# Kernel optimization log

Hardware: AMD Instinct MI355X
Metric: run time of the kernel (lower is better)

## Reference

```python
import jax, jax.numpy as jnp
import numpy as np

HEAD_DIM = 64
MASK_PENALTY = 1000000.0


def setup_inputs() -> dict:
    key = jax.random.key(0)
    kq, kk, kv, ki = jax.random.split(key, 4)
    B, H, S, D = 32, 16, 512, HEAD_DIM
    E, CAP = 8, 4  # n_experts = hidden(1024)//128, capacity per expert
    Q = jax.random.normal(kq, (B, H, S, D), dtype=jnp.float32)
    K = jax.random.normal(kk, (B, H, S, D), dtype=jnp.float32)
    V = jax.random.normal(kv, (B, H, S, D), dtype=jnp.float32)
    idx_list = jax.random.randint(ki, (E, CAP), 0, B)  # per-expert routed batch indices
    mask = jnp.ones((B, S), dtype=jnp.float32)
    return {"Q": Q, "K": K, "V": V, "idx_list": idx_list, "mask": mask}


def reference(Q, K, V, idx_list, mask):
    # Per-expert grouped attention: gather routed batch rows, QK^T, masked
    # softmax, AV. Dropout is identity in eval mode.
    scale = 1.0 / jnp.sqrt(jnp.asarray(HEAD_DIM, dtype=Q.dtype))

    def expert_attn(idx_e):
        q = Q[idx_e]            # [cap, H, S, D]
        k = K[idx_e]
        v = V[idx_e]
        m = mask[idx_e]         # [cap, S]
        dot = jnp.einsum('bhsd,bhtd->bhst', q, k) * scale
        dot = dot - MASK_PENALTY * (1.0 - m[:, None, None, :])
        p = jax.nn.softmax(dot, axis=-1)
        return jnp.einsum('bhst,bhtd->bhsd', p, v)  # [cap, H, S, D]

    X = jax.vmap(expert_attn)(idx_list)  # [E, cap, H, S, D]
    return X
```

## Files before the change

### kernel.cpp

```cpp
#include <hip/hip_runtime.h>
#include <math.h>


typedef _Float16 f16x8 __attribute__((ext_vector_type(8)));
typedef _Float16 f16x4 __attribute__((ext_vector_type(4)));
typedef _Float16 f16x2 __attribute__((ext_vector_type(2)));
typedef float    f32x4 __attribute__((ext_vector_type(4)));

#define MFMA16(a, b, c) __builtin_amdgcn_mfma_f32_16x16x32_f16((a), (b), (c), 0, 0, 0)

constexpr int Hh = 16;
constexpr int Ss = 512;
constexpr int Dd = 64;
constexpr int QB = 128;
constexpr int KVB = 64;
constexpr int NT = Ss / KVB;
constexpr float QS = 0.125f * 1.44269504088896f;
constexpr float BM = 1000000.0f * 1.44269504088896f;

union U8 { f16x8 v; f16x2 h[4]; };

__device__ __forceinline__ int SW(int row, int col) {
  return row * 64 + (col ^ ((row & 7) << 3));
}

__device__ __forceinline__ f16x2 pkrtz(float a, float b) {
  auto t = __builtin_amdgcn_cvt_pkrtz(a, b);
  return *(f16x2*)&t;
}

__global__ __launch_bounds__(256) void sparse_attn_kernel(
    const float* __restrict__ Q, const float* __restrict__ K,
    const float* __restrict__ V, const int* __restrict__ idx,
    const float* __restrict__ mask, float* __restrict__ out) {
  const int tid  = threadIdx.x;
  const int lane = tid & 63;
  const int wv   = tid >> 6;
  const int r    = lane & 15;
  const int g    = lane >> 4;

  const int phys = blockIdx.x;
  const int G    = (phys & 7) | ((phys >> 5) << 3);
  const int qb   = (phys >> 3) & 3;
  const int h    = G & 15;
  const int ec   = G >> 4;
  const int b    = idx[ec];

  __shared__ _Float16 Ks[2][64 * 64];
  __shared__ _Float16 VTs[2][64 * 64];
  __shared__ float    maskS[Ss];

  const size_t bh = ((size_t)b * Hh + h) * (size_t)Ss * Dd;
  const float* Qb = Q + bh;
  const float* Kb = K + bh;
  const float* Vb = V + bh;
  const float* mrow = mask + (size_t)b * Ss;

  *(float2*)&maskS[2 * tid] = *(const float2*)(mrow + 2 * tid);

  const int q0 = qb * QB + wv * 32;

  f16x8 qf[2][2];
#pragma unroll
  for (int mi = 0; mi < 2; ++mi)
#pragma unroll
    for (int kk = 0; kk < 2; ++kk) {
      const float* qp = Qb + (size_t)(q0 + mi * 16 + r) * Dd + kk * 32 + g * 8;
      float4 x0 = *(const float4*)qp;
      float4 x1 = *(const float4*)(qp + 4);
      U8 u;
      u.h[0] = pkrtz(x0.x * QS, x0.y * QS);
      u.h[1] = pkrtz(x0.z * QS, x0.w * QS);
      u.h[2] = pkrtz(x1.x * QS, x1.y * QS);
      u.h[3] = pkrtz(x1.z * QS, x1.w * QS);
      qf[mi][kk] = u.v;
    }

  f16x8 ones;
#pragma unroll
  for (int e = 0; e < 8; ++e) ones[e] = (_Float16)1.0f;

  f32x4 oacc[2][4];
#pragma unroll
  for (int mi = 0; mi < 2; ++mi)
#pragma unroll
    for (int nj = 0; nj < 4; ++nj) oacc[mi][nj] = (f32x4){0.f, 0.f, 0.f, 0.f};
  f32x4 lacc[2] = {(f32x4){0.f, 0.f, 0.f, 0.f}, (f32x4){0.f, 0.f, 0.f, 0.f}};

  float4 kx0[2], kx1[2];
  float  vv[2][8];

#define KV_ISSUE(KV0)                                                        \
  {                                                                          \
    _Pragma("unroll")                                                        \
    for (int it = 0; it < 2; ++it) {                                         \
      int j = it * 256 + tid;                                                \
      const float* kp_ = Kb + (size_t)((KV0) + (j >> 3)) * Dd + (j & 7) * 8; \
      kx0[it] = *(const float4*)kp_;                                         \
      kx1[it] = *(const float4*)(kp_ + 4);                                   \
    }                                                                        \
    _Pragma("unroll")                                                        \
    for (int it = 0; it < 2; ++it) {                                         \
      int oct = (tid >> 6) + 4 * it;                                         \
      int kb1 = (oct >> 2) * 16 + (oct & 3) * 4;                             \
      const float* vp = Vb + (size_t)((KV0) + kb1) * Dd + (tid & 63);        \
      _Pragma("unroll")                                                      \
      for (int jj = 0; jj < 4; ++jj) {                                       \
        vv[it][jj]     = vp[(size_t)jj * Dd];                                \
        vv[it][jj + 4] = vp[(size_t)(jj + 32) * Dd];                         \
      }                                                                      \
    }                                                                        \
  }

#define STAGE_WRITE(B)                                                       \
  {                                                                          \
    _Pragma("unroll")                                                        \
    for (int it = 0; it < 2; ++it) {                                         \
      int j = it * 256 + tid;                                                \
      U8 u;                                                                  \
      u.h[0] = pkrtz(kx0[it].x, kx0[it].y);                                  \
      u.h[1] = pkrtz(kx0[it].z, kx0[it].w);                                  \
      u.h[2] = pkrtz(kx1[it].x, kx1[it].y);                                  \
      u.h[3] = pkrtz(kx1[it].z, kx1[it].w);                                  \
      *(f16x8*)&Ks[B][SW(j >> 3, (j & 7) * 8)] = u.v;                        \
    }                                                                        \
    _Pragma("unroll")                                                        \
    for (int it = 0; it < 2; ++it) {                                         \
      int oct = (tid >> 6) + 4 * it;                                         \
      int dim = tid & 63;                                                    \
      U8 u;                                                                  \
      u.h[0] = pkrtz(vv[it][0], vv[it][1]);                                  \
      u.h[1] = pkrtz(vv[it][2], vv[it][3]);                                  \
      u.h[2] = pkrtz(vv[it][4], vv[it][5]);                                  \
      u.h[3] = pkrtz(vv[it][6], vv[it][7]);                                  \
      *(f16x8*)&VTs[B][SW(dim, oct * 8)] = u.v;                              \
    }                                                                        \
  }

  KV_ISSUE(0)
  STAGE_WRITE(0)
  __syncthreads();

  int cur = 0;
  for (int t = 0; t < NT; ++t) {
    const int kv0 = t * KVB;

    if (t < NT - 1) KV_ISSUE(kv0 + KVB)

    f32x4 bv[4];
#pragma unroll
    for (int nj = 0; nj < 4; ++nj) {
      f32x4 mv = *(const f32x4*)&maskS[kv0 + nj * 16 + g * 4];
      bv[nj][0] = mv[0] * BM - BM;
      bv[nj][1] = mv[1] * BM - BM;
      bv[nj][2] = mv[2] * BM - BM;
      bv[nj][3] = mv[3] * BM - BM;
    }

    f32x4 sf[2][4];
#pragma unroll
    for (int nj = 0; nj < 4; ++nj) { sf[0][nj] = bv[nj]; sf[1][nj] = bv[nj]; }
    __builtin_amdgcn_s_setprio(1);
#pragma unroll
    for (int nj = 0; nj < 4; ++nj)
#pragma unroll
      for (int kk = 0; kk < 2; ++kk) {
        f16x8 kf = *(const f16x8*)&Ks[cur][SW(nj * 16 + r, kk * 32 + g * 8)];
        sf[0][nj] = MFMA16(kf, qf[0][kk], sf[0][nj]);
        sf[1][nj] = MFMA16(kf, qf[1][kk], sf[1][nj]);
      }
    __builtin_amdgcn_s_setprio(0);

    f16x8 pf[2][2];
#pragma unroll
    for (int mi = 0; mi < 2; ++mi) {
      float p[4][4];
#pragma unroll
      for (int nj = 0; nj < 4; ++nj)
#pragma unroll
        for (int rg = 0; rg < 4; ++rg)
          p[nj][rg] = __builtin_amdgcn_exp2f(sf[mi][nj][rg]);
#pragma unroll
      for (int kk = 0; kk < 2; ++kk) {
        U8 u;
        u.h[0] = pkrtz(p[kk][0], p[kk][1]);
        u.h[1] = pkrtz(p[kk][2], p[kk][3]);
        u.h[2] = pkrtz(p[kk + 2][0], p[kk + 2][1]);
        u.h[3] = pkrtz(p[kk + 2][2], p[kk + 2][3]);
        pf[mi][kk] = u.v;
      }
    }

    __builtin_amdgcn_s_setprio(1);
#pragma unroll
    for (int kk = 0; kk < 2; ++kk) {
      lacc[0] = MFMA16(pf[0][kk], ones, lacc[0]);
      lacc[1] = MFMA16(pf[1][kk], ones, lacc[1]);
#pragma unroll
      for (int nj = 0; nj < 4; ++nj) {
        f16x8 vf = *(const f16x8*)&VTs[cur][SW(nj * 16 + r, kk * 32 + g * 8)];
        oacc[0][nj] = MFMA16(pf[0][kk], vf, oacc[0][nj]);
        oacc[1][nj] = MFMA16(pf[1][kk], vf, oacc[1][nj]);
      }
    }
    __builtin_amdgcn_s_setprio(0);

    if (t < NT - 1) {
      STAGE_WRITE(cur ^ 1)
      __syncthreads();
    }
    cur ^= 1;
  }

  float* ob = out + ((size_t)ec * Hh + h) * (size_t)Ss * Dd;
#pragma unroll
  for (int mi = 0; mi < 2; ++mi) {
    float i4[4];
#pragma unroll
    for (int rg = 0; rg < 4; ++rg) i4[rg] = 1.0f / lacc[mi][rg];
#pragma unroll
    for (int nj = 0; nj < 4; ++nj)
#pragma unroll
      for (int rg = 0; rg < 4; ++rg) {
        int row = q0 + mi * 16 + g * 4 + rg;
        int dim = nj * 16 + r;
        ob[(size_t)row * Dd + dim] = oacc[mi][nj][rg] * i4[rg];
      }
  }
}

extern "C" void kernel_launch(void* const* d_in, const int* in_sizes, int n_in,
                              void* d_out, int out_size, void* d_ws, size_t ws_size,
                              hipStream_t stream) {
  const float* Q    = (const float*)d_in[0];
  const float* K    = (const float*)d_in[1];
  const float* V    = (const float*)d_in[2];
  const int*   idx  = (const int*)d_in[3];
  const float* mask = (const float*)d_in[4];
  float* out = (float*)d_out;
  dim3 grid(2048), block(256);
  hipLaunchKernelGGL(sparse_attn_kernel, grid, block, 0, stream,
                     Q, K, V, idx, mask, out);
}
```

Baseline: 67.93 us.

## Use 256-row query blocks with 512 threads and single-buffered 128-row KV tiles

Each block now covers 256 query rows with 8 waves and 512 threads, so the grid halves and each K/V tile loaded from global memory is shared by twice as many queries. KV tiles grow to 128 rows and are held in a single LDS buffer. The next tile's global loads are issued into registers right after the current tile is written to LDS, and compute runs in two 64-key halves. The mask bias is precomputed once into shared memory. The cost is one extra barrier per tile, fewer blocks to spread across CUs, and higher register pressure under the 512-thread launch bound.

```diff
diff --git a/kernel.cpp b/kernel.cpp
--- a/kernel.cpp
+++ b/kernel.cpp
@@ -12,16 +12,19 @@
 constexpr int Hh = 16;
 constexpr int Ss = 512;
 constexpr int Dd = 64;
-constexpr int QB = 128;
-constexpr int KVB = 64;
-constexpr int NT = Ss / KVB;
+constexpr int QB = 256;
+constexpr int KVR = 128;
+constexpr int NR = Ss / KVR;
 constexpr float QS = 0.125f * 1.44269504088896f;
 constexpr float BM = 1000000.0f * 1.44269504088896f;
 
 union U8 { f16x8 v; f16x2 h[4]; };
 
-__device__ __forceinline__ int SW(int row, int col) {
+__device__ __forceinline__ int SW64(int row, int col) {
   return row * 64 + (col ^ ((row & 7) << 3));
+}
+__device__ __forceinline__ int SW128(int row, int col) {
+  return row * 128 + (col ^ ((row & 7) << 3));
 }
 
 __device__ __forceinline__ f16x2 pkrtz(float a, float b) {
@@ -29,7 +32,7 @@
   return *(f16x2*)&t;
 }
 
-__global__ __launch_bounds__(256) void sparse_attn_kernel(
+__global__ __launch_bounds__(512) void sparse_attn_kernel(
     const float* __restrict__ Q, const float* __restrict__ K,
     const float* __restrict__ V, const int* __restrict__ idx,
     const float* __restrict__ mask, float* __restrict__ out) {
@@ -40,15 +43,15 @@
   const int g    = lane >> 4;
 
   const int phys = blockIdx.x;
-  const int G    = (phys & 7) | ((phys >> 5) << 3);
-  const int qb   = (phys >> 3) & 3;
+  const int G    = (phys & 7) | ((phys >> 4) << 3);
+  const int qb   = (phys >> 3) & 1;
   const int h    = G & 15;
   const int ec   = G >> 4;
   const int b    = idx[ec];
 
-  __shared__ _Float16 Ks[2][64 * 64];
-  __shared__ _Float16 VTs[2][64 * 64];
-  __shared__ float    maskS[Ss];
+  __shared__ _Float16 Ks[128 * 64];
+  __shared__ _Float16 VTs[64 * 128];
+  __shared__ float    biasS[Ss];
 
   const size_t bh = ((size_t)b * Hh + h) * (size_t)Ss * Dd;
   const float* Qb = Q + bh;
@@ -56,7 +59,7 @@
   const float* Vb = V + bh;
   const float* mrow = mask + (size_t)b * Ss;
 
-  *(float2*)&maskS[2 * tid] = *(const float2*)(mrow + 2 * tid);
+  biasS[tid] = mrow[tid] * BM - BM;
 
   const int q0 = qb * QB + wv * 32;
 
@@ -94,15 +97,15 @@
   {                                                                          \
     _Pragma("unroll")                                                        \
     for (int it = 0; it < 2; ++it) {                                         \
-      int j = it * 256 + tid;                                                \
+      int j = it * 512 + tid;                                                \
       const float* kp_ = Kb + (size_t)((KV0) + (j >> 3)) * Dd + (j & 7) * 8; \
       kx0[it] = *(const float4*)kp_;                                         \
       kx1[it] = *(const float4*)(kp_ + 4);                                   \
     }                                                                        \
     _Pragma("unroll")                                                        \
     for (int it = 0; it < 2; ++it) {                                         \
-      int oct = (tid >> 6) + 4 * it;                                         \
-      int kb1 = (oct >> 2) * 16 + (oct & 3) * 4;                             \
+      int oct = tid >> 6;                                                    \
+      int kb1 = (oct >> 2) * 16 + (oct & 3) * 4 + it * 64;                   \
       const float* vp = Vb + (size_t)((KV0) + kb1) * Dd + (tid & 63);        \
       _Pragma("unroll")                                                      \
       for (int jj = 0; jj < 4; ++jj) {                                       \
@@ -112,104 +115,100 @@
     }                                                                        \
   }
 
-#define STAGE_WRITE(B)                                                       \
+#define STAGE_WRITE()                                                        \
   {                                                                          \
     _Pragma("unroll")                                                        \
     for (int it = 0; it < 2; ++it) {                                         \
-      int j = it * 256 + tid;                                                \
+      int j = it * 512 + tid;                                                \
       U8 u;                                                                  \
       u.h[0] = pkrtz(kx0[it].x, kx0[it].y);                                  \
       u.h[1] = pkrtz(kx0[it].z, kx0[it].w);                                  \
       u.h[2] = pkrtz(kx1[it].x, kx1[it].y);                                  \
       u.h[3] = pkrtz(kx1[it].z, kx1[it].w);                                  \
-      *(f16x8*)&Ks[B][SW(j >> 3, (j & 7) * 8)] = u.v;                        \
-    }                                                                        \
-    _Pragma("unroll")                                                        \
-    for (int it = 0; it < 2; ++it) {                                         \
-      int oct = (tid >> 6) + 4 * it;                                         \
+      *(f16x8*)&Ks[SW64(j >> 3, (j & 7) * 8)] = u.v;                         \
+    }                                                                        \
+    _Pragma("unroll")                                                        \
+    for (int it = 0; it < 2; ++it) {                                         \
       int dim = tid & 63;                                                    \
+      int cb  = it * 8 + (tid >> 6);                    \
       U8 u;                                                                  \
       u.h[0] = pkrtz(vv[it][0], vv[it][1]);                                  \
       u.h[1] = pkrtz(vv[it][2], vv[it][3]);                                  \
       u.h[2] = pkrtz(vv[it][4], vv[it][5]);                                  \
       u.h[3] = pkrtz(vv[it][6], vv[it][7]);                                  \
-      *(f16x8*)&VTs[B][SW(dim, oct * 8)] = u.v;                              \
+      *(f16x8*)&VTs[SW128(dim, cb * 8)] = u.v;                               \
     }                                                                        \
   }
 
   KV_ISSUE(0)
-  STAGE_WRITE(0)
-  __syncthreads();
-
-  int cur = 0;
-  for (int t = 0; t < NT; ++t) {
-    const int kv0 = t * KVB;
-
-    if (t < NT - 1) KV_ISSUE(kv0 + KVB)
-
-    f32x4 bv[4];
-#pragma unroll
-    for (int nj = 0; nj < 4; ++nj) {
-      f32x4 mv = *(const f32x4*)&maskS[kv0 + nj * 16 + g * 4];
-      bv[nj][0] = mv[0] * BM - BM;
-      bv[nj][1] = mv[1] * BM - BM;
-      bv[nj][2] = mv[2] * BM - BM;
-      bv[nj][3] = mv[3] * BM - BM;
+
+  for (int t = 0; t < NR; ++t) {
+    const int kv0 = t * KVR;
+    if (t) __syncthreads();
+
+    STAGE_WRITE()
+    if (t < NR - 1) KV_ISSUE(kv0 + KVR)
+    __syncthreads();
+
+#pragma unroll
+    for (int half = 0; half < 2; ++half) {
+      const int kh = kv0 + half * 64;
+
+      f32x4 bv[4];
+#pragma unroll
+      for (int nj = 0; nj < 4; ++nj)
+        bv[nj] = *(const f32x4*)&biasS[kh + nj * 16 + g * 4];
+
+      f32x4 sf[2][4];
+#pragma unroll
+      for (int nj = 0; nj < 4; ++nj) { sf[0][nj] = bv[nj]; sf[1][nj] = bv[nj]; }
+      __builtin_amdgcn_s_setprio(1);
+#pragma unroll
+      for (int nj = 0; nj < 4; ++nj)
+#pragma unroll
+        for (int kk = 0; kk < 2; ++kk) {
+          f16x8 kf = *(const f16x8*)&Ks[SW64(half * 64 + nj * 16 + r,
+                                             kk * 32 + g * 8)];
+          sf[0][nj] = MFMA16(kf, qf[0][kk], sf[0][nj]);
+          sf[1][nj] = MFMA16(kf, qf[1][kk], sf[1][nj]);
+        }
+      __builtin_amdgcn_s_setprio(0);
+
+      f16x8 pf[2][2];
+#pragma unroll
+      for (int mi = 0; mi < 2; ++mi) {
+        float p[4][4];
+#pragma unroll
+        for (int nj = 0; nj < 4; ++nj)
+#pragma unroll
+          for (int rg = 0; rg < 4; ++rg)
+            p[nj][rg] = __builtin_amdgcn_exp2f(sf[mi][nj][rg]);
+#pragma unroll
+        for (int kk = 0; kk < 2; ++kk) {
+          U8 u;
+          u.h[0] = pkrtz(p[kk][0], p[kk][1]);
+          u.h[1] = pkrtz(p[kk][2], p[kk][3]);
+          u.h[2] = pkrtz(p[kk + 2][0], p[kk + 2][1]);
+          u.h[3] = pkrtz(p[kk + 2][2], p[kk + 2][3]);
+          pf[mi][kk] = u.v;
+        }
+      }
+
+      __builtin_amdgcn_s_setprio(1);
+#pragma unroll
+      for (int kk = 0; kk < 2; ++kk) {
+        lacc[0] = MFMA16(pf[0][kk], ones, lacc[0]);
+        lacc[1] = MFMA16(pf[1][kk], ones, lacc[1]);
+#pragma unroll
+        for (int nj = 0; nj < 4; ++nj) {
+          f16x8 vf = *(const f16x8*)&VTs[SW128(nj * 16 + r,
+                                               half * 64 + kk * 32 + g * 8)];
+          oacc[0][nj] = MFMA16(pf[0][kk], vf, oacc[0][nj]);
+          oacc[1][nj] = MFMA16(pf[1][kk], vf, oacc[1][nj]);
+        }
+      }
+      __builtin_amdgcn_s_setprio(0);
     }
-
-    f32x4 sf[2][4];
-#pragma unroll
-    for (int nj = 0; nj < 4; ++nj) { sf[0][nj] = bv[nj]; sf[1][nj] = bv[nj]; }
-    __builtin_amdgcn_s_setprio(1);
-#pragma unroll
-    for (int nj = 0; nj < 4; ++nj)
-#pragma unroll
-      for (int kk = 0; kk < 2; ++kk) {
-        f16x8 kf = *(const f16x8*)&Ks[cur][SW(nj * 16 + r, kk * 32 + g * 8)];
-        sf[0][nj] = MFMA16(kf, qf[0][kk], sf[0][nj]);
-        sf[1][nj] = MFMA16(kf, qf[1][kk], sf[1][nj]);
-      }
-    __builtin_amdgcn_s_setprio(0);
-
-    f16x8 pf[2][2];
-#pragma unroll
-    for (int mi = 0; mi < 2; ++mi) {
-      float p[4][4];
-#pragma unroll
-      for (int nj = 0; nj < 4; ++nj)
-#pragma unroll
-        for (int rg = 0; rg < 4; ++rg)
-          p[nj][rg] = __builtin_amdgcn_exp2f(sf[mi][nj][rg]);
-#pragma unroll
-      for (int kk = 0; kk < 2; ++kk) {
-        U8 u;
-        u.h[0] = pkrtz(p[kk][0], p[kk][1]);
-        u.h[1] = pkrtz(p[kk][2], p[kk][3]);
-        u.h[2] = pkrtz(p[kk + 2][0], p[kk + 2][1]);
-        u.h[3] = pkrtz(p[kk + 2][2], p[kk + 2][3]);
-        pf[mi][kk] = u.v;
-      }
-    }
-
-    __builtin_amdgcn_s_setprio(1);
-#pragma unroll
-    for (int kk = 0; kk < 2; ++kk) {
-      lacc[0] = MFMA16(pf[0][kk], ones, lacc[0]);
-      lacc[1] = MFMA16(pf[1][kk], ones, lacc[1]);
-#pragma unroll
-      for (int nj = 0; nj < 4; ++nj) {
-        f16x8 vf = *(const f16x8*)&VTs[cur][SW(nj * 16 + r, kk * 32 + g * 8)];
-        oacc[0][nj] = MFMA16(pf[0][kk], vf, oacc[0][nj]);
-        oacc[1][nj] = MFMA16(pf[1][kk], vf, oacc[1][nj]);
-      }
-    }
-    __builtin_amdgcn_s_setprio(0);
-
-    if (t < NT - 1) {
-      STAGE_WRITE(cur ^ 1)
-      __syncthreads();
-    }
-    cur ^= 1;
   }
 
   float* ob = out + ((size_t)ec * Hh + h) * (size_t)Ss * Dd;
@@ -238,7 +237,7 @@
   const int*   idx  = (const int*)d_in[3];
   const float* mask = (const float*)d_in[4];
   float* out = (float*)d_out;
-  dim3 grid(2048), block(256);
+  dim3 grid(1024), block(512);
   hipLaunchKernelGGL(sparse_attn_kernel, grid, block, 0, stream,
                      Q, K, V, idx, mask, out);
 }
```

Measured after the change: 66.16 us. -2.6%, faster.

## Single-buffer K/V LDS tiles with staggered K and V prefetch stages

Applied to the files above, without the earlier changes.

Replaces the double-buffered K and V^T shared-memory tiles with single buffers. K and V global loads and LDS writes are now split and staggered: V for the current tile is staged at loop start while K for the next tile is staged after the PV step, with an added barrier between QK and PV. The mask bias is precomputed once into shared memory instead of being recomputed per tile. This halves the tile LDS footprint, which may allow more resident blocks, at the cost of an extra block-wide synchronization per iteration and less overlap slack.

```diff
diff --git a/kernel.cpp b/kernel.cpp
--- a/kernel.cpp
+++ b/kernel.cpp
@@ -3,7 +3,6 @@
 
 
 typedef _Float16 f16x8 __attribute__((ext_vector_type(8)));
-typedef _Float16 f16x4 __attribute__((ext_vector_type(4)));
 typedef _Float16 f16x2 __attribute__((ext_vector_type(2)));
 typedef float    f32x4 __attribute__((ext_vector_type(4)));
 
@@ -46,9 +45,9 @@
   const int ec   = G >> 4;
   const int b    = idx[ec];
 
-  __shared__ _Float16 Ks[2][64 * 64];
-  __shared__ _Float16 VTs[2][64 * 64];
-  __shared__ float    maskS[Ss];
+  __shared__ _Float16 Ks[64 * 64];
+  __shared__ _Float16 VTs[64 * 64];
+  __shared__ float    biasS[Ss];
 
   const size_t bh = ((size_t)b * Hh + h) * (size_t)Ss * Dd;
   const float* Qb = Q + bh;
@@ -56,7 +55,11 @@
   const float* Vb = V + bh;
   const float* mrow = mask + (size_t)b * Ss;
 
-  *(float2*)&maskS[2 * tid] = *(const float2*)(mrow + 2 * tid);
+  {
+    float2 m2 = *(const float2*)(mrow + 2 * tid);
+    biasS[2 * tid]     = m2.x * BM - BM;
+    biasS[2 * tid + 1] = m2.y * BM - BM;
+  }
 
   const int q0 = qb * QB + wv * 32;
 
@@ -90,7 +93,7 @@
   float4 kx0[2], kx1[2];
   float  vv[2][8];
 
-#define KV_ISSUE(KV0)                                                        \
+#define K_ISSUE(KV0)                                                         \
   {                                                                          \
     _Pragma("unroll")                                                        \
     for (int it = 0; it < 2; ++it) {                                         \
@@ -99,6 +102,10 @@
       kx0[it] = *(const float4*)kp_;                                         \
       kx1[it] = *(const float4*)(kp_ + 4);                                   \
     }                                                                        \
+  }
+
+#define V_ISSUE(KV0)                                                         \
+  {                                                                          \
     _Pragma("unroll")                                                        \
     for (int it = 0; it < 2; ++it) {                                         \
       int oct = (tid >> 6) + 4 * it;                                         \
@@ -112,7 +119,7 @@
     }                                                                        \
   }
 
-#define STAGE_WRITE(B)                                                       \
+#define STAGE_K()                                                            \
   {                                                                          \
     _Pragma("unroll")                                                        \
     for (int it = 0; it < 2; ++it) {                                         \
@@ -122,54 +129,53 @@
       u.h[1] = pkrtz(kx0[it].z, kx0[it].w);                                  \
       u.h[2] = pkrtz(kx1[it].x, kx1[it].y);                                  \
       u.h[3] = pkrtz(kx1[it].z, kx1[it].w);                                  \
-      *(f16x8*)&Ks[B][SW(j >> 3, (j & 7) * 8)] = u.v;                        \
-    }                                                                        \
+      *(f16x8*)&Ks[SW(j >> 3, (j & 7) * 8)] = u.v;                           \
+    }                                                                        \
+  }
+
+#define STAGE_V()                                                            \
+  {                                                                          \
     _Pragma("unroll")                                                        \
     for (int it = 0; it < 2; ++it) {                                         \
       int oct = (tid >> 6) + 4 * it;                                         \
-      int dim = tid & 63;                                                    \
-      U8 u;                                                                  \
-      u.h[0] = pkrtz(vv[it][0], vv[it][1]);                                  \
-      u.h[1] = pkrtz(vv[it][2], vv[it][3]);                                  \
-      u.h[2] = pkrtz(vv[it][4], vv[it][5]);                                  \
-      u.h[3] = pkrtz(vv[it][6], vv[it][7]);                                  \
-      *(f16x8*)&VTs[B][SW(dim, oct * 8)] = u.v;                              \
-    }                                                                        \
-  }
-
-  KV_ISSUE(0)
-  STAGE_WRITE(0)
+      U8 u2;                                                                 \
+      u2.h[0] = pkrtz(vv[it][0], vv[it][1]);                                 \
+      u2.h[1] = pkrtz(vv[it][2], vv[it][3]);                                 \
+      u2.h[2] = pkrtz(vv[it][4], vv[it][5]);                                 \
+      u2.h[3] = pkrtz(vv[it][6], vv[it][7]);                                 \
+      *(f16x8*)&VTs[SW(tid & 63, oct * 8)] = u2.v;                           \
+    }                                                                        \
+  }
+
+  K_ISSUE(0)
+  V_ISSUE(0)
+  STAGE_K()
+  K_ISSUE(KVB)
   __syncthreads();
 
-  int cur = 0;
   for (int t = 0; t < NT; ++t) {
     const int kv0 = t * KVB;
 
-    if (t < NT - 1) KV_ISSUE(kv0 + KVB)
-
-    f32x4 bv[4];
+    STAGE_V()
+    if (t < NT - 1) V_ISSUE(kv0 + KVB)
+
+    f32x4 sf[2][4];
 #pragma unroll
     for (int nj = 0; nj < 4; ++nj) {
-      f32x4 mv = *(const f32x4*)&maskS[kv0 + nj * 16 + g * 4];
-      bv[nj][0] = mv[0] * BM - BM;
-      bv[nj][1] = mv[1] * BM - BM;
-      bv[nj][2] = mv[2] * BM - BM;
-      bv[nj][3] = mv[3] * BM - BM;
-    }
-
-    f32x4 sf[2][4];
-#pragma unroll
-    for (int nj = 0; nj < 4; ++nj) { sf[0][nj] = bv[nj]; sf[1][nj] = bv[nj]; }
+      f32x4 bv = *(const f32x4*)&biasS[kv0 + nj * 16 + g * 4];
+      sf[0][nj] = bv; sf[1][nj] = bv;
+    }
     __builtin_amdgcn_s_setprio(1);
 #pragma unroll
     for (int nj = 0; nj < 4; ++nj)
 #pragma unroll
       for (int kk = 0; kk < 2; ++kk) {
-        f16x8 kf = *(const f16x8*)&Ks[cur][SW(nj * 16 + r, kk * 32 + g * 8)];
+        f16x8 kf = *(const f16x8*)&Ks[SW(nj * 16 + r, kk * 32 + g * 8)];
         sf[0][nj] = MFMA16(kf, qf[0][kk], sf[0][nj]);
         sf[1][nj] = MFMA16(kf, qf[1][kk], sf[1][nj]);
       }
     __builtin_amdgcn_s_setprio(0);
+    __syncthreads();
 
     f16x8 pf[2][2];
 #pragma unroll
@@ -198,7 +204,7 @@
       lacc[1] = MFMA16(pf[1][kk], ones, lacc[1]);
 #pragma unroll
       for (int nj = 0; nj < 4; ++nj) {
-        f16x8 vf = *(const f16x8*)&VTs[cur][SW(nj * 16 + r, kk * 32 + g * 8)];
+        f16x8 vf = *(const f16x8*)&VTs[SW(nj * 16 + r, kk * 32 + g * 8)];
         oacc[0][nj] = MFMA16(pf[0][kk], vf, oacc[0][nj]);
         oacc[1][nj] = MFMA16(pf[1][kk], vf, oacc[1][nj]);
       }
@@ -206,10 +212,10 @@
     __builtin_amdgcn_s_setprio(0);
 
     if (t < NT - 1) {
-      STAGE_WRITE(cur ^ 1)
+      STAGE_K()
+      if (t < NT - 2) K_ISSUE(kv0 + 2 * KVB)
       __syncthreads();
     }
-    cur ^= 1;
   }
 
   float* ob = out + ((size_t)ec * Hh + h) * (size_t)Ss * Dd;
```

Result: faster. 65.75 us (-3.2%).
